# Kernel tuning notes

Hardware: AMD Instinct MI355X
Metric: run time of the kernel (lower is better)

The kernel has to match this reference:

```python
import jax, jax.numpy as jnp
import numpy as np

B, S, D = 2, 2048, 1024
H = 16
HD = D // H  # 64


def setup_inputs() -> dict:
    key = jax.random.key(0)
    ks = jax.random.split(key, 5)
    scale = 1.0 / np.sqrt(D)
    return {
        "x": jax.random.normal(ks[0], (B, S, D), dtype=jnp.float32),
        "kqv_w": jax.random.normal(ks[1], (3 * D, D), dtype=jnp.float32) * scale,
        "kqv_b": jnp.zeros((3 * D,), dtype=jnp.float32),
        "out_w": jax.random.normal(ks[2], (D, D), dtype=jnp.float32) * scale,
        "out_b": jnp.zeros((D,), dtype=jnp.float32),
    }


def reference(x, kqv_w, kqv_b, out_w, out_b):
    # x: [B, S, D] -> torch code transposes to [S, B, D] (seq-first)
    xs = jnp.transpose(x, (1, 0, 2))  # [S, B, D]
    qkv = xs @ kqv_w.T + kqv_b        # [S, B, 3D]
    q, k, v = jnp.split(qkv, 3, axis=-1)  # each [S, B, D]

    def to_heads(t):
        # [S, B, D] -> [S, B*H, HD] -> [B*H, S, HD]
        return jnp.transpose(t.reshape(S, B * H, HD), (1, 0, 2))

    q, k, v = to_heads(q), to_heads(k), to_heads(v)
    # NOTE: original module computes self.scaling but never applies it -> no q scaling.
    attn = jnp.einsum('nqd,nkd->nqk', q, k)      # [B*H, S, S]
    attn = jax.nn.softmax(attn, axis=-1)
    out = jnp.einsum('nqk,nkd->nqd', attn, v)    # [B*H, S, HD]
    out = jnp.transpose(out, (1, 0, 2)).reshape(S, B, D)  # [S, B, D]
    out = out @ out_w.T + out_b
    return jnp.transpose(out, (1, 0, 2))  # [B, S, D]
```

## Files before the change

kernel.cpp:

```cpp
#include <hip/hip_runtime.h>

#define SEQ   2048
#define DIM   1024
#define NH    16
#define HD    64
#define BH    32
#define TOK   4096

typedef __bf16 bf16;
typedef __attribute__((ext_vector_type(4))) __bf16 bf16x4;
typedef __attribute__((ext_vector_type(8))) __bf16 bf16x8;
typedef __attribute__((ext_vector_type(4))) float f32x4;

#define LOG2E 1.44269504f

__device__ inline f32x4 mfma16(bf16x8 a, bf16x8 b, f32x4 c) {
  return __builtin_amdgcn_mfma_f32_16x16x32_bf16(a, b, c, 0, 0, 0);
}

__device__ inline void gload_lds16(const bf16* g, bf16* lds) {
  __builtin_amdgcn_global_load_lds(
      (const __attribute__((address_space(1))) void*)g,
      (__attribute__((address_space(3))) void*)lds, 16, 0, 0);
}

__device__ inline float exp2_hw(float x) {
  float r;
  asm("v_exp_f32 %0, %1" : "=v"(r) : "v"(x));
  return r;
}

__device__ inline void split8(const float* src, bf16x8& hi, bf16x8& lo) {
  float4 a = *(const float4*)src;
  float4 b = *(const float4*)(src + 4);
  float f[8] = {a.x, a.y, a.z, a.w, b.x, b.y, b.z, b.w};
#pragma unroll
  for (int i = 0; i < 8; ++i) {
    bf16 h = (bf16)f[i];
    hi[i] = h;
    lo[i] = (bf16)(f[i] - (float)h);
  }
}

__device__ inline void cast8(const float* src, bf16* dst) {
  float4 a = *(const float4*)src;
  float4 b = *(const float4*)(src + 4);
  bf16x8 v;
  v[0] = (bf16)a.x; v[1] = (bf16)a.y; v[2] = (bf16)a.z; v[3] = (bf16)a.w;
  v[4] = (bf16)b.x; v[5] = (bf16)b.y; v[6] = (bf16)b.z; v[7] = (bf16)b.w;
  *(bf16x8*)dst = v;
}

__global__ void prep_kernel(const float* __restrict__ x,
                            const float* __restrict__ kqv_w,
                            const float* __restrict__ out_w,
                            bf16* __restrict__ xh, bf16* __restrict__ xl,
                            bf16* __restrict__ wbf, bf16* __restrict__ wout) {
  const int NX8 = TOK * DIM / 8;
  const int NW8 = 3 * DIM * DIM / 8;
  const int NO8 = DIM * DIM / 8;
  int i = blockIdx.x * 256 + threadIdx.x;
  if (i < NX8) {
    bf16x8 h, l;
    split8(x + (size_t)i * 8, h, l);
    ((bf16x8*)xh)[i] = h;
    ((bf16x8*)xl)[i] = l;
  } else if (i < NX8 + NW8) {
    int j = i - NX8;
    cast8(kqv_w + (size_t)j * 8, wbf + (size_t)j * 8);
  } else if (i < NX8 + NW8 + NO8) {
    int j = i - NX8 - NW8;
    cast8(out_w + (size_t)j * 8, wout + (size_t)j * 8);
  }
}

__global__ __launch_bounds__(256) void gemm_qkv_ps(
    const bf16* __restrict__ xh, const bf16* __restrict__ xl,
    const bf16* __restrict__ wbf, const float* __restrict__ bias,
    bf16* __restrict__ qhh, bf16* __restrict__ qhl, bf16* __restrict__ kh,
    bf16* __restrict__ vP) {
  __shared__ bf16 AhA[64 * 64], AlA[64 * 64], BhA[64 * 64];
  __shared__ bf16 AhB[64 * 64], AlB[64 * 64], BhB[64 * 64];
  const int tid = threadIdx.x;
  const int lane = tid & 63;
  const int wave = tid >> 6;
  const int lr = lane & 15, lk = lane >> 4;
  const int bid = blockIdx.x;
  const int swz = (bid & 7) * 96 + (bid >> 3);
  const int m0 = (swz / 24) * 128, n0 = (swz % 24) * 128;
  const bool two_term = (n0 < DIM);
  const int wm = (wave >> 1) * 64, wn = (wave & 1) * 64;
  f32x4 acc[4][4] = {};

  const int c0i = tid, c1i = 256 + tid;
  const int rp0 = c0i >> 3, lc0 = (c0i & 7) ^ (rp0 & 7);
  const int mm0 = (lc0 >> 2) * 64 + rp0, kk0 = (lc0 & 3) * 8;
  const int rp1 = c1i >> 3, lc1 = (c1i & 7) ^ (rp1 & 7);
  const int mm1 = (lc1 >> 2) * 64 + rp1, kk1 = (lc1 & 3) * 8;
  const bf16* pA0 = xh + (size_t)(m0 + mm0) * DIM + kk0;
  const bf16* pA1 = xh + (size_t)(m0 + mm1) * DIM + kk1;
  const bf16* pL0 = xl + (size_t)(m0 + mm0) * DIM + kk0;
  const bf16* pL1 = xl + (size_t)(m0 + mm1) * DIM + kk1;
  const bf16* pB0 = wbf + (size_t)(n0 + mm0) * DIM + kk0;
  const bf16* pB1 = wbf + (size_t)(n0 + mm1) * DIM + kk1;

  auto stageG = [&](bf16* Ah_, bf16* Al_, bf16* Bh_) {
    gload_lds16(pA0, Ah_ + c0i * 8);
    gload_lds16(pA1, Ah_ + c1i * 8);
    if (two_term) {
      gload_lds16(pL0, Al_ + c0i * 8);
      gload_lds16(pL1, Al_ + c1i * 8);
    }
    gload_lds16(pB0, Bh_ + c0i * 8);
    gload_lds16(pB1, Bh_ + c1i * 8);
    pA0 += 32; pA1 += 32; pL0 += 32; pL1 += 32;
    pB0 += 32; pB1 += 32;
  };

  auto computeG = [&](const bf16* Ah, const bf16* Al, const bf16* Bh) {
    bf16x8 afh[4], afl[4], bfv[4];
#pragma unroll
    for (int i = 0; i < 4; ++i) {
      int m = wm + i * 16 + lr;
      int rp = m & 63;
      int pc = ((m >> 6) * 4 + lk) ^ (rp & 7);
      afh[i] = *(const bf16x8*)(Ah + rp * 64 + pc * 8);
    }
#pragma unroll
    for (int j = 0; j < 4; ++j) {
      int m = wn + j * 16 + lr;
      int rp = m & 63;
      int pc = ((m >> 6) * 4 + lk) ^ (rp & 7);
      bfv[j] = *(const bf16x8*)(Bh + rp * 64 + pc * 8);
    }
    __builtin_amdgcn_s_setprio(1);
#pragma unroll
    for (int i = 0; i < 4; ++i)
#pragma unroll
      for (int j = 0; j < 4; ++j)
        acc[i][j] = mfma16(afh[i], bfv[j], acc[i][j]);
    __builtin_amdgcn_s_setprio(0);
    if (two_term) {
#pragma unroll
      for (int i = 0; i < 4; ++i) {
        int m = wm + i * 16 + lr;
        int rp = m & 63;
        int pc = ((m >> 6) * 4 + lk) ^ (rp & 7);
        afl[i] = *(const bf16x8*)(Al + rp * 64 + pc * 8);
      }
      __builtin_amdgcn_s_setprio(1);
#pragma unroll
      for (int i = 0; i < 4; ++i)
#pragma unroll
        for (int j = 0; j < 4; ++j)
          acc[i][j] = mfma16(afl[i], bfv[j], acc[i][j]);
      __builtin_amdgcn_s_setprio(0);
    }
  };

  stageG(AhA, AlA, BhA);
  __syncthreads();
  for (int k0 = 0; k0 < DIM; k0 += 64) {
    stageG(AhB, AlB, BhB);
    computeG(AhA, AlA, BhA);
    __syncthreads();
    if (k0 + 64 < DIM) {
      stageG(AhA, AlA, BhA);
    }
    computeG(AhB, AlB, BhB);
    __syncthreads();
  }

#pragma unroll
  for (int j = 0; j < 4; ++j) {
    int col = n0 + wn + j * 16 + lr;
    float bv = bias[col];
    int part = col >> 10, cc2 = col & 1023;
    int h = cc2 >> 6, d = cc2 & 63;
#pragma unroll
    for (int i = 0; i < 4; ++i) {
      int rowb = m0 + wm + i * 16 + lk * 4;
#pragma unroll
      for (int r = 0; r < 4; ++r) {
        int row = rowb + r;
        float val = acc[i][j][r] + bv;
        int b = row >> 11, s = row & 2047;
        int n = b * NH + h;
        size_t idx = ((size_t)n * SEQ + s) * HD + d;
        if (part == 0) {
          float vq = val * LOG2E;
          bf16 qh_ = (bf16)vq;
          qhh[idx] = qh_;
          qhl[idx] = (bf16)(vq - (float)qh_);
        } else if (part == 1) {
          kh[idx] = (bf16)val;
        } else {
          int kt = s >> 6;
          int s6 = s & 63;
          int p = (s6 >> 5) & 1;
          int s5 = s6 & 31;
          int hh = s5 >> 4, l = (s5 >> 2) & 3, rr = s5 & 3;
          int u = (p * 4 + l) * 8 + hh * 4 + rr;
          vP[(((size_t)n * 32 + kt) * 64 + d) * 64 + u] = (bf16)val;
        }
      }
    }
  }
}

__global__ __launch_bounds__(256) void gemm_out(
    const bf16* __restrict__ A, const bf16* __restrict__ Bw,
    const float* __restrict__ bias, float* __restrict__ outF) {
  __shared__ bf16 AsA[64 * 64], BsA[64 * 64];
  __shared__ bf16 AsB[64 * 64], BsB[64 * 64];
  const int tid = threadIdx.x;
  const int lane = tid & 63;
  const int wave = tid >> 6;
  const int lr = lane & 15, lk = lane >> 4;
  const int bid = blockIdx.x;
  const int swz = (bid & 7) * 32 + (bid >> 3);
  const int m0 = (swz >> 3) * 128, n0 = (swz & 7) * 128;
  const int wm = (wave >> 1) * 64, wn = (wave & 1) * 64;
  f32x4 acc[4][4] = {};

  const int c0i = tid, c1i = 256 + tid;
  const int rp0 = c0i >> 3, lc0 = (c0i & 7) ^ (rp0 & 7);
  const int mm0 = (lc0 >> 2) * 64 + rp0, kk0 = (lc0 & 3) * 8;
  const int rp1 = c1i >> 3, lc1 = (c1i & 7) ^ (rp1 & 7);
  const int mm1 = (lc1 >> 2) * 64 + rp1, kk1 = (lc1 & 3) * 8;
  const bf16* pA0 = A + (size_t)(m0 + mm0) * DIM + kk0;
  const bf16* pA1 = A + (size_t)(m0 + mm1) * DIM + kk1;
  const bf16* pB0 = Bw + (size_t)(n0 + mm0) * DIM + kk0;
  const bf16* pB1 = Bw + (size_t)(n0 + mm1) * DIM + kk1;

#define STAGEO(As_, Bs_)              \
  do {                                \
    gload_lds16(pA0, As_ + c0i * 8);  \
    gload_lds16(pA1, As_ + c1i * 8);  \
    gload_lds16(pB0, Bs_ + c0i * 8);  \
    gload_lds16(pB1, Bs_ + c1i * 8);  \
    pA0 += 32; pA1 += 32;             \
    pB0 += 32; pB1 += 32;             \
  } while (0)

  auto computeO = [&](const bf16* As, const bf16* Bs) {
    bf16x8 af[4], bfv[4];
#pragma unroll
    for (int i = 0; i < 4; ++i) {
      int m = wm + i * 16 + lr;
      int rp = m & 63;
      int pc = ((m >> 6) * 4 + lk) ^ (rp & 7);
      af[i] = *(const bf16x8*)(As + rp * 64 + pc * 8);
    }
#pragma unroll
    for (int j = 0; j < 4; ++j) {
      int m = wn + j * 16 + lr;
      int rp = m & 63;
      int pc = ((m >> 6) * 4 + lk) ^ (rp & 7);
      bfv[j] = *(const bf16x8*)(Bs + rp * 64 + pc * 8);
    }
    __builtin_amdgcn_s_setprio(1);
#pragma unroll
    for (int i = 0; i < 4; ++i)
#pragma unroll
      for (int j = 0; j < 4; ++j)
        acc[i][j] = mfma16(af[i], bfv[j], acc[i][j]);
    __builtin_amdgcn_s_setprio(0);
  };

  STAGEO(AsA, BsA);
  __syncthreads();
  for (int k0 = 0; k0 < DIM; k0 += 64) {
    STAGEO(AsB, BsB);
    computeO(AsA, BsA);
    __syncthreads();
    if (k0 + 64 < DIM) {
      STAGEO(AsA, BsA);
    }
    computeO(AsB, BsB);
    __syncthreads();
  }
#undef STAGEO

#pragma unroll
  for (int j = 0; j < 4; ++j) {
    int col = n0 + wn + j * 16 + lr;
    float bv = bias[col];
#pragma unroll
    for (int i = 0; i < 4; ++i) {
      int rowb = m0 + wm + i * 16 + lk * 4;
#pragma unroll
      for (int r = 0; r < 4; ++r)
        outF[(size_t)(rowb + r) * DIM + col] = acc[i][j][r] + bv;
    }
  }
}

__global__ __launch_bounds__(256) void attn_kernel(
    const bf16* __restrict__ qhh, const bf16* __restrict__ qhl,
    const bf16* __restrict__ kh, const bf16* __restrict__ vP,
    bf16* __restrict__ aout) {
  __shared__ bf16 KsA[64 * 64], VsA[64 * 64];
  __shared__ bf16 KsB[64 * 64], VsB[64 * 64];
  const int tid = threadIdx.x;
  const int lane = tid & 63;
  const int w = tid >> 6;
  const int lr = lane & 15, lk = lane >> 4;
  const int bid = blockIdx.x;
  const int swz = (bid & 7) * 64 + (bid >> 3);
  const int n = swz >> 4;
  const int q0 = (swz & 15) * 128 + w * 32;

  const bf16* qbh = qhh + ((size_t)n * SEQ + q0) * HD;
  const bf16* qbl = qhl + ((size_t)n * SEQ + q0) * HD;
  bf16x8 aqh[2][2], aql[2][2];
#pragma unroll
  for (int g = 0; g < 2; ++g) {
    aqh[g][0] = *(const bf16x8*)(qbh + (g * 16 + lr) * HD + lk * 8);
    aqh[g][1] = *(const bf16x8*)(qbh + (g * 16 + lr) * HD + 32 + lk * 8);
    aql[g][0] = *(const bf16x8*)(qbl + (g * 16 + lr) * HD + lk * 8);
    aql[g][1] = *(const bf16x8*)(qbl + (g * 16 + lr) * HD + 32 + lk * 8);
  }

  const int c0i = tid, c1i = 256 + tid;
  const int r0 = c0i >> 3, lc0 = ((c0i & 7) ^ (r0 & 7)) * 8;
  const int r1 = c1i >> 3, lc1 = ((c1i & 7) ^ (r1 & 7)) * 8;
  const size_t kbase = (size_t)n * SEQ * HD;
  const bf16* pK0 = kh + kbase + (size_t)r0 * HD + lc0;
  const bf16* pK1 = kh + kbase + (size_t)r1 * HD + lc1;
  const bf16* pV0 = vP + kbase + (size_t)r0 * 64 + lc0;
  const bf16* pV1 = vP + kbase + (size_t)r1 * 64 + lc1;

  bf16x8 ones;
#pragma unroll
  for (int i = 0; i < 8; ++i) ones[i] = (bf16)1.0f;

  f32x4 o[2][4] = {};
  float lrow[2][4] = {};

#define STAGE(Ks_, Vs_)                   \
  do {                                    \
    gload_lds16(pK0, Ks_ + c0i * 8);      \
    gload_lds16(pK1, Ks_ + c1i * 8);      \
    gload_lds16(pV0, Vs_ + c0i * 8);      \
    gload_lds16(pV1, Vs_ + c1i * 8);      \
    pK0 += 64 * HD; pK1 += 64 * HD;       \
    pV0 += 64 * 64; pV1 += 64 * 64;       \
  } while (0)

  auto compute = [&](const bf16* Ks, const bf16* Vs) {
    f32x4 sa[2][4] = {};
    __builtin_amdgcn_s_setprio(1);
#pragma unroll
    for (int j = 0; j < 4; ++j) {
      int row = j * 16 + lr;
      int c0 = (lk ^ (row & 7)) * 8;
      int c1 = ((4 + lk) ^ (row & 7)) * 8;
      const bf16* kr = Ks + row * 64;
      bf16x8 b0 = *(const bf16x8*)(kr + c0);
      bf16x8 b1 = *(const bf16x8*)(kr + c1);
#pragma unroll
      for (int g = 0; g < 2; ++g) {
        sa[g][j] = mfma16(b0, aqh[g][0], sa[g][j]);
        sa[g][j] = mfma16(b1, aqh[g][1], sa[g][j]);
        sa[g][j] = mfma16(b0, aql[g][0], sa[g][j]);
        sa[g][j] = mfma16(b1, aql[g][1], sa[g][j]);
      }
    }
    __builtin_amdgcn_s_setprio(0);

    bf16x8 pa[2][2];
#pragma unroll
    for (int g = 0; g < 2; ++g)
#pragma unroll
      for (int jj = 0; jj < 2; ++jj)
#pragma unroll
        for (int r = 0; r < 4; ++r) {
          pa[g][0][jj * 4 + r] = (bf16)exp2_hw(sa[g][jj][r]);
          pa[g][1][jj * 4 + r] = (bf16)exp2_hw(sa[g][2 + jj][r]);
        }

    __builtin_amdgcn_s_setprio(1);
    f32x4 ls[2] = {};
#pragma unroll
    for (int g = 0; g < 2; ++g) {
      ls[g] = mfma16(pa[g][0], ones, ls[g]);
      ls[g] = mfma16(pa[g][1], ones, ls[g]);
    }
#pragma unroll
    for (int dj = 0; dj < 4; ++dj) {
      int row = dj * 16 + lr;
      const bf16* vr = Vs + row * 64;
#pragma unroll
      for (int p = 0; p < 2; ++p) {
        bf16x8 vf = *(const bf16x8*)(vr + (((p * 4 + lk) ^ (row & 7)) * 8));
#pragma unroll
        for (int g = 0; g < 2; ++g)
          o[g][dj] = mfma16(pa[g][p], vf, o[g][dj]);
      }
    }
    __builtin_amdgcn_s_setprio(0);
#pragma unroll
    for (int g = 0; g < 2; ++g)
#pragma unroll
      for (int r = 0; r < 4; ++r) lrow[g][r] += ls[g][r];
  };

  STAGE(KsA, VsA);
  __syncthreads();

  for (int it = 0; it < SEQ / 64; it += 2) {
    STAGE(KsB, VsB);
    compute(KsA, VsA);
    __syncthreads();
    if (it + 2 < SEQ / 64) {
      STAGE(KsA, VsA);
    }
    compute(KsB, VsB);
    __syncthreads();
  }
#undef STAGE

  const int b = n >> 4, h = n & 15;
#pragma unroll
  for (int g = 0; g < 2; ++g)
#pragma unroll
    for (int r = 0; r < 4; ++r) {
      float inv = 1.0f / lrow[g][r];
      int s = q0 + g * 16 + lk * 4 + r;
      size_t base = ((size_t)(b * SEQ + s)) * DIM + h * HD;
#pragma unroll
      for (int j = 0; j < 4; ++j)
        aout[base + j * 16 + lr] = (bf16)(o[g][j][r] * inv);
    }
}

extern "C" void kernel_launch(void* const* d_in, const int* in_sizes, int n_in,
                              void* d_out, int out_size, void* d_ws, size_t ws_size,
                              hipStream_t stream) {
  const float* x     = (const float*)d_in[0];
  const float* kqv_w = (const float*)d_in[1];
  const float* kqv_b = (const float*)d_in[2];
  const float* out_w = (const float*)d_in[3];
  const float* out_b = (const float*)d_in[4];
  float* out = (float*)d_out;

  const size_t NX  = (size_t)TOK * DIM;
  const size_t NW  = (size_t)3 * DIM * DIM;
  const size_t NO  = (size_t)DIM * DIM;
  const size_t NKV = (size_t)BH * SEQ * HD;

  bf16* xh   = (bf16*)d_ws;
  bf16* xl   = xh + NX;
  bf16* wbf  = xl + NX;
  bf16* wout = wbf + NW;
  bf16* qhh  = wout + NO;
  bf16* qhl  = qhh + NKV;
  bf16* kh   = qhl + NKV;
  bf16* vP   = kh + NKV;
  bf16* aout = xh;

  const int PREP_BLOCKS = (int)((NX + NW + NO) / 8 / 256);
  prep_kernel<<<PREP_BLOCKS, 256, 0, stream>>>(x, kqv_w, out_w, xh, xl, wbf, wout);
  gemm_qkv_ps<<<768, 256, 0, stream>>>(xh, xl, wbf, kqv_b, qhh, qhl, kh, vP);
  attn_kernel<<<512, 256, 0, stream>>>(qhh, qhl, kh, vP, aout);
  gemm_out<<<256, 256, 0, stream>>>(aout, wout, out_b, out);
}
```

Baseline: 132.9 us.

## Split attention KV range across two wave groups per block and reduce in LDS

Doubles the attention block to 512 threads. Two groups of four waves each process half of the key/value sequence for the same query tile, then combine their partial outputs and row sums through shared memory before normalizing. This halves each wave's serial KV loop and doubles the waves available for latency hiding. The cost is doubled LDS per block, which may limit occupancy, plus an extra LDS reduction and barrier at the end.

Measured after the change: 129.2 us (median of 2 runs). 2.8% less time.

```diff
diff --git a/kernel.cpp b/kernel.cpp
--- a/kernel.cpp
+++ b/kernel.cpp
@@ -296,20 +296,27 @@
   }
 }
 
-__global__ __launch_bounds__(256) void attn_kernel(
+__global__ __launch_bounds__(512) void attn_kernel(
     const bf16* __restrict__ qhh, const bf16* __restrict__ qhl,
     const bf16* __restrict__ kh, const bf16* __restrict__ vP,
     bf16* __restrict__ aout) {
-  __shared__ bf16 KsA[64 * 64], VsA[64 * 64];
-  __shared__ bf16 KsB[64 * 64], VsB[64 * 64];
+  __shared__ bf16 smem[8 * 4096];
   const int tid = threadIdx.x;
   const int lane = tid & 63;
   const int w = tid >> 6;
+  const int G = w >> 2;
+  const int wsub = w & 3;
   const int lr = lane & 15, lk = lane >> 4;
   const int bid = blockIdx.x;
   const int swz = (bid & 7) * 64 + (bid >> 3);
   const int n = swz >> 4;
-  const int q0 = (swz & 15) * 128 + w * 32;
+  const int q0 = (swz & 15) * 128 + wsub * 32;
+  const int kv0 = G * (SEQ / 2);
+
+  bf16* KsA = smem + ((0 * 2 + G) * 2 + 0) * 4096;
+  bf16* VsA = smem + ((0 * 2 + G) * 2 + 1) * 4096;
+  bf16* KsB = smem + ((1 * 2 + G) * 2 + 0) * 4096;
+  bf16* VsB = smem + ((1 * 2 + G) * 2 + 1) * 4096;
 
   const bf16* qbh = qhh + ((size_t)n * SEQ + q0) * HD;
   const bf16* qbl = qhl + ((size_t)n * SEQ + q0) * HD;
@@ -322,14 +329,15 @@
     aql[g][1] = *(const bf16x8*)(qbl + (g * 16 + lr) * HD + 32 + lk * 8);
   }
 
-  const int c0i = tid, c1i = 256 + tid;
+  const int gtid = tid & 255;
+  const int c0i = gtid, c1i = 256 + gtid;
   const int r0 = c0i >> 3, lc0 = ((c0i & 7) ^ (r0 & 7)) * 8;
   const int r1 = c1i >> 3, lc1 = ((c1i & 7) ^ (r1 & 7)) * 8;
   const size_t kbase = (size_t)n * SEQ * HD;
-  const bf16* pK0 = kh + kbase + (size_t)r0 * HD + lc0;
-  const bf16* pK1 = kh + kbase + (size_t)r1 * HD + lc1;
-  const bf16* pV0 = vP + kbase + (size_t)r0 * 64 + lc0;
-  const bf16* pV1 = vP + kbase + (size_t)r1 * 64 + lc1;
+  const bf16* pK0 = kh + kbase + (size_t)(kv0 + r0) * HD + lc0;
+  const bf16* pK1 = kh + kbase + (size_t)(kv0 + r1) * HD + lc1;
+  const bf16* pV0 = vP + kbase + (size_t)(kv0 + r0) * 64 + lc0;
+  const bf16* pV1 = vP + kbase + (size_t)(kv0 + r1) * 64 + lc1;
 
   bf16x8 ones;
 #pragma unroll
@@ -409,11 +417,11 @@
   STAGE(KsA, VsA);
   __syncthreads();
 
-  for (int it = 0; it < SEQ / 64; it += 2) {
+  for (int it = 0; it < SEQ / 128; it += 2) {
     STAGE(KsB, VsB);
     compute(KsA, VsA);
     __syncthreads();
-    if (it + 2 < SEQ / 64) {
+    if (it + 2 < SEQ / 128) {
       STAGE(KsA, VsA);
     }
     compute(KsB, VsB);
@@ -421,18 +429,51 @@
   }
 #undef STAGE
 
-  const int b = n >> 4, h = n & 15;
-#pragma unroll
-  for (int g = 0; g < 2; ++g)
-#pragma unroll
-    for (int r = 0; r < 4; ++r) {
-      float inv = 1.0f / lrow[g][r];
-      int s = q0 + g * 16 + lk * 4 + r;
-      size_t base = ((size_t)(b * SEQ + s)) * DIM + h * HD;
-#pragma unroll
-      for (int j = 0; j < 4; ++j)
-        aout[base + j * 16 + lr] = (bf16)(o[g][j][r] * inv);
-    }
+  float* xb = (float*)smem;
+  if (G == 1) {
+    float* p = xb + gtid * 41;
+#pragma unroll
+    for (int g = 0; g < 2; ++g)
+#pragma unroll
+      for (int dj = 0; dj < 4; ++dj)
+#pragma unroll
+        for (int i = 0; i < 4; ++i)
+          p[(g * 4 + dj) * 4 + i] = o[g][dj][i];
+#pragma unroll
+    for (int g = 0; g < 2; ++g)
+#pragma unroll
+      for (int r = 0; r < 4; ++r)
+        p[32 + g * 4 + r] = lrow[g][r];
+  }
+  __syncthreads();
+  if (G == 0) {
+    float* p = xb + gtid * 41;
+#pragma unroll
+    for (int g = 0; g < 2; ++g)
+#pragma unroll
+      for (int dj = 0; dj < 4; ++dj)
+#pragma unroll
+        for (int i = 0; i < 4; ++i)
+          o[g][dj][i] += p[(g * 4 + dj) * 4 + i];
+#pragma unroll
+    for (int g = 0; g < 2; ++g)
+#pragma unroll
+      for (int r = 0; r < 4; ++r)
+        lrow[g][r] += p[32 + g * 4 + r];
+
+    const int b = n >> 4, h = n & 15;
+#pragma unroll
+    for (int g = 0; g < 2; ++g)
+#pragma unroll
+      for (int r = 0; r < 4; ++r) {
+        float inv = 1.0f / lrow[g][r];
+        int s = q0 + g * 16 + lk * 4 + r;
+        size_t base = ((size_t)(b * SEQ + s)) * DIM + h * HD;
+#pragma unroll
+        for (int j = 0; j < 4; ++j)
+          aout[base + j * 16 + lr] = (bf16)(o[g][j][r] * inv);
+      }
+  }
 }
 
 extern "C" void kernel_launch(void* const* d_in, const int* in_sizes, int n_in,
@@ -463,6 +504,6 @@
   const int PREP_BLOCKS = (int)((NX + NW + NO) / 8 / 256);
   prep_kernel<<<PREP_BLOCKS, 256, 0, stream>>>(x, kqv_w, out_w, xh, xl, wbf, wout);
   gemm_qkv_ps<<<768, 256, 0, stream>>>(xh, xl, wbf, kqv_b, qhh, qhl, kh, vP);
-  attn_kernel<<<512, 256, 0, stream>>>(qhh, qhl, kh, vP, aout);
+  attn_kernel<<<512, 512, 0, stream>>>(qhh, qhl, kh, vP, aout);
   gemm_out<<<256, 256, 0, stream>>>(aout, wout, out_b, out);
 }
```
